# Performance work log

Hardware: AMD Instinct MI355X
Metric: run time of the kernel (lower is better)

Reference implementation:

```python
import math
import jax, jax.numpy as jnp
import numpy as np

NUM_HEADS = 12
NUM_LANDMARKS = 32

def iterative_inv(mat, n_iter=6):
    # mat: [B, H, m, m] row-stochastic kernel; Newton-Schulz pseudo-inverse
    m = mat.shape[-1]
    I = jnp.eye(m, dtype=mat.dtype)
    K = mat
    # 'else' branch: per-(B,H) normalization by max column sum
    denom = jnp.max(jnp.sum(K, axis=-2), axis=-1)[..., None, None]
    V = jnp.swapaxes(K, -1, -2) / denom
    for _ in range(n_iter):
        KV = jnp.matmul(K, V)
        V = jnp.matmul(0.25 * V, 13.0 * I - jnp.matmul(KV, 15.0 * I - jnp.matmul(KV, 7.0 * I - KV)))
    return V

def setup_inputs() -> dict:
    key = jax.random.key(0)
    k1, k2, k3 = jax.random.split(key, 3)
    B, N, C = 8, 2048, 768
    x = jax.random.normal(k1, (B, N, C), dtype=jnp.float32)
    w_qkv = jax.random.normal(k2, (C, 3 * C), dtype=jnp.float32) * (1.0 / math.sqrt(C))
    w_proj = jax.random.normal(k3, (C, C), dtype=jnp.float32) * (1.0 / math.sqrt(C))
    b_proj = jnp.zeros((C,), dtype=jnp.float32)
    return {"x": x, "w_qkv": w_qkv, "w_proj": w_proj, "b_proj": b_proj}

def reference(x, w_qkv, w_proj, b_proj):
    B, N, C = x.shape
    H = NUM_HEADS
    d = C // H
    m = NUM_LANDMARKS
    qkv = (x @ w_qkv).reshape(B, N, 3, H, d).transpose(2, 0, 3, 1, 4)  # [3,B,H,N,d]
    Q, K, V = qkv[0], qkv[1], qkv[2]
    scale = 1.0 / math.sqrt(math.sqrt(d))
    Q = Q * scale
    K = K * scale
    # landmark pooling: mean over contiguous chunks of size N//m
    Q_l = Q.reshape(B, H, m, N // m, d).mean(axis=-2)  # [B,H,m,d]
    K_l = K.reshape(B, H, m, N // m, d).mean(axis=-2)
    kernel_1 = jax.nn.softmax(jnp.einsum('bhnd,bhmd->bhnm', Q, K_l), axis=-1)   # [B,H,N,m]
    kernel_2 = jax.nn.softmax(jnp.einsum('bhmd,bhkd->bhmk', Q_l, K_l), axis=-1) # [B,H,m,m]
    kernel_3 = jax.nn.softmax(jnp.einsum('bhmd,bhnd->bhmn', Q_l, K), axis=-1)   # [B,H,m,N]
    X = jnp.matmul(jnp.matmul(kernel_1, iterative_inv(kernel_2)), jnp.matmul(kernel_3, V))  # [B,H,N,d]
    X = X.transpose(0, 2, 1, 3).reshape(B, N, C)
    return X @ w_proj + b_proj
```

## Files before the change

kernel.cpp:

```cpp
#include <hip/hip_runtime.h>
#include <hip/hip_bf16.h>

typedef __hip_bfloat16 bf16;
typedef __attribute__((ext_vector_type(8))) __bf16 bf16x8;
typedef __attribute__((ext_vector_type(4))) float f32x4;

#define NB 8
#define SEQ 2048
#define CH 768
#define NH 12
#define HD 64
#define NL 32
#define BHT (NB*NH)
#define TOK (NB*SEQ)
#define QK_SCALE 0.35355339059327379f

__device__ __forceinline__ void async_ld16(const bf16* g, bf16* l) {
    unsigned loff = (unsigned)__builtin_amdgcn_readfirstlane((int)(unsigned)(uintptr_t)l);
    __builtin_amdgcn_global_load_lds(
        (const __attribute__((address_space(1))) unsigned*)(uintptr_t)g,
        (__attribute__((address_space(3))) unsigned*)(uintptr_t)loff, 16, 0, 0);
}

__global__ void convert_x(const float* __restrict__ x, bf16* __restrict__ xb) {
    size_t i = ((size_t)blockIdx.x * 256 + threadIdx.x) * 8;
    float4 a = *reinterpret_cast<const float4*>(x + i);
    float4 b = *reinterpret_cast<const float4*>(x + i + 4);
    alignas(16) bf16 tmp[8];
    tmp[0] = __float2bfloat16(a.x); tmp[1] = __float2bfloat16(a.y);
    tmp[2] = __float2bfloat16(a.z); tmp[3] = __float2bfloat16(a.w);
    tmp[4] = __float2bfloat16(b.x); tmp[5] = __float2bfloat16(b.y);
    tmp[6] = __float2bfloat16(b.z); tmp[7] = __float2bfloat16(b.w);
    *reinterpret_cast<uint4*>(xb + i) = *reinterpret_cast<const uint4*>(tmp);
}

__global__ void transpose_f32(const float* __restrict__ in, bf16* __restrict__ outp,
                              int Hrows, int Wcols) {
    __shared__ float tile[32][33];
    int bx = blockIdx.x * 32, by = blockIdx.y * 32;
    int tx = threadIdx.x, ty = threadIdx.y;
    for (int i = 0; i < 32; i += 8)
        tile[ty + i][tx] = in[(size_t)(by + ty + i) * Wcols + bx + tx];
    __syncthreads();
    for (int i = 0; i < 32; i += 8)
        outp[(size_t)(bx + ty + i) * Hrows + by + tx] = __float2bfloat16(tile[tx][ty + i]);
}

template <int EPI>
__global__ __launch_bounds__(256) void gemm_bt(
    const bf16* __restrict__ A, const bf16* __restrict__ Bt,
    int Nout, int Kdim,
    bf16* __restrict__ q, bf16* __restrict__ k, bf16* __restrict__ vt,
    float* __restrict__ Ql, float* __restrict__ Kl,
    float* __restrict__ outp, const float* __restrict__ bias_f) {
    __shared__ __align__(16) bf16 As[128 * 32];
    __shared__ __align__(16) bf16 Bs[128 * 32];
    const int t = threadIdx.x;
    const int wave = t >> 6, lane = t & 63;
    const int quad = lane >> 4, l15 = lane & 15;
    const int wr = wave >> 1, wc = wave & 1;

    int p = blockIdx.y * gridDim.x + blockIdx.x;
    int xcd = p & 7, j = p >> 3;
    int gx = gridDim.x;
    int bn = j % gx;
    int bm = (j / gx) * 8 + xcd;
    const int bm0 = bm * 128;
    const int bn0 = bn * 128;

    f32x4 acc[4][4];
    const f32x4 zero4 = {0.f, 0.f, 0.f, 0.f};
    for (int i = 0; i < 4; i++)
        for (int jj = 0; jj < 4; jj++) acc[i][jj] = zero4;

    const int sw = (quad ^ (l15 & 3)) * 8;

    for (int k0 = 0; k0 < Kdim; k0 += 32) {
        __syncthreads();
        #pragma unroll
        for (int r = 0; r < 2; r++) {
            int c = t + r * 256;
            int row = c >> 2;
            int chunk = ((c & 3) ^ (row & 3)) * 8;
            async_ld16(&A[(size_t)(bm0 + row) * Kdim + k0 + chunk], &As[(wave * 64 + r * 256) * 8]);
            async_ld16(&Bt[(size_t)(bn0 + row) * Kdim + k0 + chunk], &Bs[(wave * 64 + r * 256) * 8]);
        }
        __syncthreads();
        bf16x8 af[4], bfr[4];
        #pragma unroll
        for (int mi = 0; mi < 4; mi++)
            af[mi] = *reinterpret_cast<const bf16x8*>(&As[(wr * 64 + mi * 16 + l15) * 32 + sw]);
        #pragma unroll
        for (int ni = 0; ni < 4; ni++)
            bfr[ni] = *reinterpret_cast<const bf16x8*>(&Bs[(wc * 64 + ni * 16 + l15) * 32 + sw]);
        #pragma unroll
        for (int mi = 0; mi < 4; mi++)
            #pragma unroll
            for (int ni = 0; ni < 4; ni++)
                acc[mi][ni] = __builtin_amdgcn_mfma_f32_16x16x32_bf16(af[mi], bfr[ni], acc[mi][ni], 0, 0, 0);
    }

    if (EPI == 0) {
        const int which = bn0 / CH;
        const int rem0 = bn0 - which * CH + wc * 64;
        const int b = bm0 >> 11;
        const int nnb = (bm0 & 2047) + wr * 64;
        if (which < 2) {
            bf16* dstqk = (which == 0) ? q : k;
            float* dstl = (which == 0) ? Ql : Kl;
            const int l = nnb >> 6;
            #pragma unroll
            for (int ni = 0; ni < 4; ni++) {
                int rem = rem0 + ni * 16 + l15;
                int h = rem >> 6, dd = rem & 63;
                int bh = b * NH + h;
                float colsum = 0.f;
                #pragma unroll
                for (int mi = 0; mi < 4; mi++) {
                    int nn0 = nnb + mi * 16 + quad * 4;
                    #pragma unroll
                    for (int r = 0; r < 4; r++) {
                        float val = acc[mi][ni][r];
                        colsum += val;
                        dstqk[((size_t)bh * SEQ + nn0 + r) * HD + dd] = __float2bfloat16(val * QK_SCALE);
                    }
                }
                colsum += __shfl_xor(colsum, 16);
                colsum += __shfl_xor(colsum, 32);
                if (quad == 0)
                    dstl[((size_t)bh * NL + l) * HD + dd] = colsum * (QK_SCALE / 64.f);
            }
        } else {
            #pragma unroll
            for (int ni = 0; ni < 4; ni++) {
                int rem = rem0 + ni * 16 + l15;
                int h = rem >> 6, dd = rem & 63;
                int bh = b * NH + h;
                #pragma unroll
                for (int mi = 0; mi < 4; mi++) {
                    int nn0 = nnb + mi * 16 + quad * 4;
                    alignas(8) bf16 four[4];
                    #pragma unroll
                    for (int r = 0; r < 4; r++) four[r] = __float2bfloat16(acc[mi][ni][r]);
                    *reinterpret_cast<uint2*>(&vt[((size_t)bh * HD + dd) * SEQ + nn0]) =
                        *reinterpret_cast<const uint2*>(four);
                }
            }
        }
    } else {
        #pragma unroll
        for (int mi = 0; mi < 4; mi++)
            #pragma unroll
            for (int ni = 0; ni < 4; ni++) {
                int col = bn0 + wc * 64 + ni * 16 + l15;
                #pragma unroll
                for (int r = 0; r < 4; r++) {
                    int row = bm0 + wr * 64 + mi * 16 + quad * 4 + r;
                    outp[(size_t)row * Nout + col] = acc[mi][ni][r] + bias_f[col];
                }
            }
    }
}

__global__ __launch_bounds__(256) void k3_pv(const float* __restrict__ Ql,
                                             const bf16* __restrict__ Kb,
                                             const bf16* __restrict__ Vt,
                                             float* __restrict__ Opart,
                                             float* __restrict__ Spart) {
    __shared__ __align__(16) bf16 Pw[4][32 * 136];
    __shared__ __align__(16) float Ored[4][32 * 65];
    __shared__ float Sred[4 * 32];
    const int bh = blockIdx.x, cc = blockIdx.y;
    const int n0 = cc * 512;
    const int t = threadIdx.x;
    const int w = t >> 6, lane = t & 63;
    const int quad = lane >> 4, l15 = lane & 15;

    const bf16* Kbh = Kb + (size_t)bh * SEQ * HD;
    const bf16* Vtb = Vt + (size_t)bh * HD * SEQ;

    bf16x8 af[2][2];
    #pragma unroll
    for (int mt = 0; mt < 2; mt++)
        #pragma unroll
        for (int kh = 0; kh < 2; kh++) {
            const float* src = Ql + (size_t)bh * NL * HD + (mt * 16 + l15) * 64 + kh * 32 + quad * 8;
            alignas(16) bf16 tmp[8];
            #pragma unroll
            for (int jj = 0; jj < 8; jj++) tmp[jj] = __float2bfloat16(src[jj]);
            af[mt][kh] = *reinterpret_cast<const bf16x8*>(tmp);
        }

    const f32x4 zero4 = {0.f, 0.f, 0.f, 0.f};
    f32x4 oacc[2][4];
    #pragma unroll
    for (int mt = 0; mt < 2; mt++)
        #pragma unroll
        for (int nd = 0; nd < 4; nd++) oacc[mt][nd] = zero4;
    float rs[2][4];
    #pragma unroll
    for (int mt = 0; mt < 2; mt++)
        #pragma unroll
        for (int r = 0; r < 4; r++) rs[mt][r] = 0.f;

    bf16* Pme = &Pw[w][0];

    #pragma unroll
    for (int h = 0; h < 2; h++) {
        f32x4 sacc[2][4];
        #pragma unroll
        for (int mt = 0; mt < 2; mt++)
            #pragma unroll
            for (int nt = 0; nt < 4; nt++) sacc[mt][nt] = zero4;
        #pragma unroll
        for (int nt = 0; nt < 4; nt++) {
            int n = n0 + w * 128 + h * 64 + nt * 16 + l15;
            bf16x8 kf0 = *reinterpret_cast<const bf16x8*>(&Kbh[(size_t)n * HD + quad * 8]);
            bf16x8 kf1 = *reinterpret_cast<const bf16x8*>(&Kbh[(size_t)n * HD + 32 + quad * 8]);
            #pragma unroll
            for (int mt = 0; mt < 2; mt++) {
                sacc[mt][nt] = __builtin_amdgcn_mfma_f32_16x16x32_bf16(af[mt][0], kf0, sacc[mt][nt], 0, 0, 0);
                sacc[mt][nt] = __builtin_amdgcn_mfma_f32_16x16x32_bf16(af[mt][1], kf1, sacc[mt][nt], 0, 0, 0);
            }
        }
        #pragma unroll
        for (int mt = 0; mt < 2; mt++)
            #pragma unroll
            for (int nt = 0; nt < 4; nt++)
                #pragma unroll
                for (int r = 0; r < 4; r++) {
                    float pv = __expf(sacc[mt][nt][r]);
                    rs[mt][r] += pv;
                    int row = mt * 16 + quad * 4 + r;
                    Pme[row * 136 + h * 64 + nt * 16 + l15] = __float2bfloat16(pv);
                }
    }
    __asm__ __volatile__("s_waitcnt lgkmcnt(0)" ::: "memory");

    #pragma unroll
    for (int kt = 0; kt < 4; kt++) {
        bf16x8 pa[2];
        pa[0] = *reinterpret_cast<const bf16x8*>(&Pme[l15 * 136 + kt * 32 + quad * 8]);
        pa[1] = *reinterpret_cast<const bf16x8*>(&Pme[(16 + l15) * 136 + kt * 32 + quad * 8]);
        int kbase = n0 + w * 128 + kt * 32 + quad * 8;
        #pragma unroll
        for (int nd = 0; nd < 4; nd++) {
            bf16x8 bv = *reinterpret_cast<const bf16x8*>(&Vtb[(size_t)(nd * 16 + l15) * SEQ + kbase]);
            oacc[0][nd] = __builtin_amdgcn_mfma_f32_16x16x32_bf16(pa[0], bv, oacc[0][nd], 0, 0, 0);
            oacc[1][nd] = __builtin_amdgcn_mfma_f32_16x16x32_bf16(pa[1], bv, oacc[1][nd], 0, 0, 0);
        }
    }

    #pragma unroll
    for (int mt = 0; mt < 2; mt++)
        #pragma unroll
        for (int r = 0; r < 4; r++) {
            float v = rs[mt][r];
            #pragma unroll
            for (int o = 1; o < 16; o <<= 1) v += __shfl_xor(v, o);
            rs[mt][r] = v;
        }
    if (l15 == 0)
        #pragma unroll
        for (int mt = 0; mt < 2; mt++)
            #pragma unroll
            for (int r = 0; r < 4; r++)
                Sred[w * 32 + mt * 16 + quad * 4 + r] = rs[mt][r];
    #pragma unroll
    for (int mt = 0; mt < 2; mt++)
        #pragma unroll
        for (int nd = 0; nd < 4; nd++)
            #pragma unroll
            for (int r = 0; r < 4; r++)
                Ored[w][(mt * 16 + quad * 4 + r) * 65 + nd * 16 + l15] = oacc[mt][nd][r];
    __syncthreads();

    float* Op = Opart + ((size_t)bh * 4 + cc) * (NL * HD);
    for (int e = t; e < 2048; e += 256) {
        int m = e >> 6, dd = e & 63;
        Op[e] = Ored[0][m * 65 + dd] + Ored[1][m * 65 + dd] +
                Ored[2][m * 65 + dd] + Ored[3][m * 65 + dd];
    }
    if (t < 32)
        Spart[((size_t)bh * 4 + cc) * NL + t] = Sred[t] + Sred[32 + t] + Sred[64 + t] + Sred[96 + t];
}

__device__ inline void mm32(float* Cm, const float* Am, const float* Bm, int t) {
    for (int e = t; e < 1024; e += 256) {
        int i = e >> 5, jj = e & 31;
        float s = 0.f;
        #pragma unroll
        for (int kk = 0; kk < 32; kk++) s += Am[i * 32 + kk] * Bm[kk * 32 + jj];
        Cm[e] = s;
    }
}

__global__ __launch_bounds__(256) void newton_inv(const float* __restrict__ Ql,
                                                  const float* __restrict__ Kl,
                                                  const float* __restrict__ Opart,
                                                  const float* __restrict__ Spart,
                                                  float* __restrict__ W2) {
    __shared__ float K2[1024], Vv[1024], KV[1024], Ta[1024], Tb[1024];
    __shared__ float K3[2048];
    __shared__ float stot[32];
    __shared__ float red[32];
    __shared__ float denom_s;
    int bh = blockIdx.x;
    int t = threadIdx.x;
    const float* ql = Ql + (size_t)bh * NL * HD;
    const float* kl = Kl + (size_t)bh * NL * HD;

    if (t < 32) {
        const float* sp = Spart + (size_t)bh * 4 * NL;
        stot[t] = sp[t] + sp[32 + t] + sp[64 + t] + sp[96 + t];
    }
    {
        const float* op = Opart + (size_t)bh * 4 * (NL * HD);
        for (int e = t; e < 2048; e += 256)
            K3[e] = op[e] + op[2048 + e] + op[4096 + e] + op[6144 + e];
    }

    for (int e = t; e < 1024; e += 256) {
        int i = e >> 5, jj = e & 31;
        float s = 0.f;
        #pragma unroll 8
        for (int d = 0; d < 64; d++) s += ql[i * 64 + d] * kl[jj * 64 + d];
        K2[e] = s;
    }
    __syncthreads();
    for (int e = t; e < 2048; e += 256) K3[e] *= (1.f / stot[e >> 6]);
    if (t < 32) {
        float mx = -1e30f;
        for (int jj = 0; jj < 32; jj++) mx = fmaxf(mx, K2[t * 32 + jj]);
        float sm = 0.f;
        for (int jj = 0; jj < 32; jj++) { float e = __expf(K2[t * 32 + jj] - mx); K2[t * 32 + jj] = e; sm += e; }
        float inv = 1.f / sm;
        for (int jj = 0; jj < 32; jj++) K2[t * 32 + jj] *= inv;
    }
    __syncthreads();
    if (t < 32) {
        float cs = 0.f;
        for (int i = 0; i < 32; i++) cs += K2[i * 32 + t];
        red[t] = cs;
    }
    __syncthreads();
    if (t == 0) {
        float mx = red[0];
        for (int jj = 1; jj < 32; jj++) mx = fmaxf(mx, red[jj]);
        denom_s = mx;
    }
    __syncthreads();
    float invden = 1.f / denom_s;
    for (int e = t; e < 1024; e += 256) {
        int i = e >> 5, jj = e & 31;
        Vv[e] = K2[jj * 32 + i] * invden;
    }
    __syncthreads();
    for (int it = 0; it < 6; it++) {
        mm32(KV, K2, Vv, t);
        __syncthreads();
        for (int e = t; e < 1024; e += 256) { int i = e >> 5, jj = e & 31; Ta[e] = ((i == jj) ? 7.f : 0.f) - KV[e]; }
        __syncthreads();
        mm32(Tb, KV, Ta, t);
        __syncthreads();
        for (int e = t; e < 1024; e += 256) { int i = e >> 5, jj = e & 31; Tb[e] = ((i == jj) ? 15.f : 0.f) - Tb[e]; }
        __syncthreads();
        mm32(Ta, KV, Tb, t);
        __syncthreads();
        for (int e = t; e < 1024; e += 256) { int i = e >> 5, jj = e & 31; Ta[e] = ((i == jj) ? 13.f : 0.f) - Ta[e]; }
        __syncthreads();
        mm32(Tb, Vv, Ta, t);
        __syncthreads();
        for (int e = t; e < 1024; e += 256) Vv[e] = 0.25f * Tb[e];
        __syncthreads();
    }
    for (int e = t; e < 2048; e += 256) {
        int i = e >> 6, dd = e & 63;
        float s = 0.f;
        #pragma unroll
        for (int kk = 0; kk < 32; kk++) s += Vv[i * 32 + kk] * K3[kk * 64 + dd];
        W2[(size_t)bh * NL * HD + e] = s;
    }
}

__global__ __launch_bounds__(256) void rows_fused(const bf16* __restrict__ Qb,
                                                  const float* __restrict__ Kl,
                                                  const float* __restrict__ W2,
                                                  bf16* __restrict__ Xp) {
    __shared__ __align__(16) bf16 Klb[32 * 64];
    __shared__ __align__(16) bf16 W2t[64 * 32];
    __shared__ __align__(16) bf16 Pw[4][32 * 40];
    const int bh = blockIdx.x, tile = blockIdx.y;
    const int t = threadIdx.x, w = t >> 6, lane = t & 63;
    const int quad = lane >> 4, l15 = lane & 15;

    {
        const float* ksrc = Kl + (size_t)bh * NL * HD;
        const float* wsrc = W2 + (size_t)bh * NL * HD;
        int e0 = t * 8;
        #pragma unroll
        for (int jj = 0; jj < 8; jj++) {
            int e = e0 + jj;
            Klb[e] = __float2bfloat16(ksrc[e]);
            int kk = e >> 6, dd = e & 63;
            W2t[dd * 32 + kk] = __float2bfloat16(wsrc[e]);
        }
    }
    __syncthreads();

    const int b = bh / NH, h = bh - b * NH;
    const int row0 = tile * 128 + w * 32;
    const bf16* qbase = Qb + ((size_t)bh * SEQ + row0) * HD;

    const f32x4 zero4 = {0.f, 0.f, 0.f, 0.f};
    f32x4 sacc[2][2];
    #pragma unroll
    for (int mt = 0; mt < 2; mt++)
        #pragma unroll
        for (int nt = 0; nt < 2; nt++) sacc[mt][nt] = zero4;
    #pragma unroll
    for (int kh = 0; kh < 2; kh++) {
        bf16x8 bk0 = *reinterpret_cast<const bf16x8*>(&Klb[(l15) * 64 + kh * 32 + quad * 8]);
        bf16x8 bk1 = *reinterpret_cast<const bf16x8*>(&Klb[(16 + l15) * 64 + kh * 32 + quad * 8]);
        #pragma unroll
        for (int mt = 0; mt < 2; mt++) {
            bf16x8 aq = *reinterpret_cast<const bf16x8*>(&qbase[(size_t)(mt * 16 + l15) * HD + kh * 32 + quad * 8]);
            sacc[mt][0] = __builtin_amdgcn_mfma_f32_16x16x32_bf16(aq, bk0, sacc[mt][0], 0, 0, 0);
            sacc[mt][1] = __builtin_amdgcn_mfma_f32_16x16x32_bf16(aq, bk1, sacc[mt][1], 0, 0, 0);
        }
    }

    float invs[2][4];
    bf16* Pme = &Pw[w][0];
    #pragma unroll
    for (int mt = 0; mt < 2; mt++)
        #pragma unroll
        for (int r = 0; r < 4; r++) {
            float v0 = __expf(sacc[mt][0][r]);
            float v1 = __expf(sacc[mt][1][r]);
            int row = mt * 16 + quad * 4 + r;
            Pme[row * 40 + l15] = __float2bfloat16(v0);
            Pme[row * 40 + 16 + l15] = __float2bfloat16(v1);
            float v = v0 + v1;
            #pragma unroll
            for (int o = 1; o < 16; o <<= 1) v += __shfl_xor(v, o);
            invs[mt][r] = 1.f / v;
        }
    __asm__ __volatile__("s_waitcnt lgkmcnt(0)" ::: "memory");

    f32x4 oacc[2][4];
    #pragma unroll
    for (int mt = 0; mt < 2; mt++)
        #pragma unroll
        for (int nd = 0; nd < 4; nd++) oacc[mt][nd] = zero4;
    bf16x8 pa[2];
    pa[0] = *reinterpret_cast<const bf16x8*>(&Pme[l15 * 40 + quad * 8]);
    pa[1] = *reinterpret_cast<const bf16x8*>(&Pme[(16 + l15) * 40 + quad * 8]);
    #pragma unroll
    for (int nd = 0; nd < 4; nd++) {
        bf16x8 bw = *reinterpret_cast<const bf16x8*>(&W2t[(nd * 16 + l15) * 32 + quad * 8]);
        oacc[0][nd] = __builtin_amdgcn_mfma_f32_16x16x32_bf16(pa[0], bw, oacc[0][nd], 0, 0, 0);
        oacc[1][nd] = __builtin_amdgcn_mfma_f32_16x16x32_bf16(pa[1], bw, oacc[1][nd], 0, 0, 0);
    }

    #pragma unroll
    for (int mt = 0; mt < 2; mt++)
        #pragma unroll
        for (int nd = 0; nd < 4; nd++)
            #pragma unroll
            for (int r = 0; r < 4; r++) {
                int row = row0 + mt * 16 + quad * 4 + r;
                Xp[((size_t)(b * SEQ + row)) * CH + h * 64 + nd * 16 + l15] =
                    __float2bfloat16(oacc[mt][nd][r] * invs[mt][r]);
            }
}

extern "C" void kernel_launch(void* const* d_in, const int* in_sizes, int n_in,
                              void* d_out, int out_size, void* d_ws, size_t ws_size,
                              hipStream_t stream) {
    const float* x      = (const float*)d_in[0];
    const float* w_qkv  = (const float*)d_in[1];
    const float* w_proj = (const float*)d_in[2];
    const float* b_proj = (const float*)d_in[3];
    float* out = (float*)d_out;

    char* ws = (char*)d_ws;
    size_t off = 0;
    auto alloc = [&](size_t bytes) -> void* {
        void* p = ws + off;
        off += (bytes + 255) & ~(size_t)255;
        return p;
    };
    bf16* wqkvT  = (bf16*)alloc((size_t)3 * CH * CH * 2);
    bf16* wprojT = (bf16*)alloc((size_t)CH * CH * 2);
    bf16* Qb     = (bf16*)alloc((size_t)BHT * SEQ * HD * 2);
    bf16* Kb     = (bf16*)alloc((size_t)BHT * SEQ * HD * 2);
    bf16* Vt     = (bf16*)alloc((size_t)BHT * SEQ * HD * 2);
    float* Ql    = (float*)alloc((size_t)BHT * NL * HD * 4);
    float* Kl    = (float*)alloc((size_t)BHT * NL * HD * 4);
    float* Opart = (float*)alloc((size_t)BHT * 4 * NL * HD * 4);
    float* Spart = (float*)alloc((size_t)BHT * 4 * NL * 4);
    float* W2    = (float*)alloc((size_t)BHT * NL * HD * 4);
    bf16* Xp     = (bf16*)alloc((size_t)TOK * CH * 2);
    if (ws_size < off) return;
    bf16* xb = Xp;

    convert_x<<<TOK * CH / 2048, 256, 0, stream>>>(x, xb);
    transpose_f32<<<dim3((3 * CH) / 32, CH / 32), dim3(32, 8), 0, stream>>>(w_qkv, wqkvT, CH, 3 * CH);
    transpose_f32<<<dim3(CH / 32, CH / 32), dim3(32, 8), 0, stream>>>(w_proj, wprojT, CH, CH);

    gemm_bt<0><<<dim3((3 * CH) / 128, TOK / 128), 256, 0, stream>>>(
        xb, wqkvT, 3 * CH, CH, Qb, Kb, Vt, Ql, Kl, nullptr, nullptr);

    k3_pv<<<dim3(BHT, 4), 256, 0, stream>>>(Ql, Kb, Vt, Opart, Spart);
    newton_inv<<<BHT, 256, 0, stream>>>(Ql, Kl, Opart, Spart, W2);
    rows_fused<<<dim3(BHT, SEQ / 128), 256, 0, stream>>>(Qb, Kl, W2, Xp);

    gemm_bt<1><<<dim3(CH / 128, TOK / 128), 256, 0, stream>>>(
        Xp, wprojT, CH, CH, nullptr, nullptr, nullptr, nullptr, nullptr, out, b_proj);
}
```

Measured before the change: 282.0 us.

## Rewrite GEMM as 256x256 tile, 8-wave, double-buffered pipelined kernel

Replaces the 128x128 single-buffered GEMM (BK=32) with a 256x256 tile, 512-thread, BK=64 kernel. It double-buffers LDS with async global-to-LDS loads staged in quarters interleaved with MFMA phases, uses s_setprio around the MFMA blocks, and adds an 8-way XOR swizzle. The goal is to hide load latency and improve data reuse for both the QKV and projection GEMMs. The cost is heavy register and LDS use (128KB LDS) and far fewer blocks: the projection GEMM gets only 3x64 = 192 blocks, which may underfill the 256 CUs.

```diff
diff --git a/kernel.cpp b/kernel.cpp
--- a/kernel.cpp
+++ b/kernel.cpp
@@ -14,6 +14,10 @@
 #define BHT (NB*NH)
 #define TOK (NB*SEQ)
 #define QK_SCALE 0.35355339059327379f
+
+#define BAR() __builtin_amdgcn_s_barrier()
+#define WLGKM0() __asm__ __volatile__("s_waitcnt lgkmcnt(0)" ::: "memory")
+#define WVM(n) __asm__ __volatile__("s_waitcnt vmcnt(" #n ")" ::: "memory")
 
 __device__ __forceinline__ void async_ld16(const bf16* g, bf16* l) {
     unsigned loff = (unsigned)__builtin_amdgcn_readfirstlane((int)(unsigned)(uintptr_t)l);
@@ -47,97 +51,192 @@
 }
 
 template <int EPI>
-__global__ __launch_bounds__(256) void gemm_bt(
+__global__ __launch_bounds__(512, 2) void gemm_bt(
     const bf16* __restrict__ A, const bf16* __restrict__ Bt,
     int Nout, int Kdim,
     bf16* __restrict__ q, bf16* __restrict__ k, bf16* __restrict__ vt,
     float* __restrict__ Ql, float* __restrict__ Kl,
     float* __restrict__ outp, const float* __restrict__ bias_f) {
-    __shared__ __align__(16) bf16 As[128 * 32];
-    __shared__ __align__(16) bf16 Bs[128 * 32];
+    __shared__ __align__(16) bf16 As[2][256 * 64];
+    __shared__ __align__(16) bf16 Bs[2][256 * 64];
     const int t = threadIdx.x;
     const int wave = t >> 6, lane = t & 63;
     const int quad = lane >> 4, l15 = lane & 15;
-    const int wr = wave >> 1, wc = wave & 1;
+    const int wr = wave >> 2, wc = wave & 3;
 
     int p = blockIdx.y * gridDim.x + blockIdx.x;
     int xcd = p & 7, j = p >> 3;
     int gx = gridDim.x;
     int bn = j % gx;
     int bm = (j / gx) * 8 + xcd;
-    const int bm0 = bm * 128;
-    const int bn0 = bn * 128;
-
-    f32x4 acc[4][4];
+    const int bm0 = bm * 256;
+    const int bn0 = bn * 256;
+
+    const int T = Kdim >> 6;
+
+    const int srow = t >> 3;
+    const int scol = (((t & 7) ^ (srow & 7)) << 3);
+    const bf16* Abase = A + (size_t)(bm0 + srow) * Kdim + scol;
+    const bf16* Bbase = Bt + (size_t)(bn0 + srow) * Kdim + scol;
+
+    auto stageA = [&](int kt, int hf) {
+        const bf16* g = Abase + (size_t)(hf * 128) * Kdim + kt * 64;
+        bf16* l = &As[kt & 1][hf * 8192 + t * 8];
+        async_ld16(g, l);
+        async_ld16(g + (size_t)64 * Kdim, l + 4096);
+    };
+    auto stageB = [&](int kt, int hf) {
+        const bf16* g = Bbase + (size_t)(hf * 128) * Kdim + kt * 64;
+        bf16* l = &Bs[kt & 1][hf * 8192 + t * 8];
+        async_ld16(g, l);
+        async_ld16(g + (size_t)64 * Kdim, l + 4096);
+    };
+
+    const int swk[2] = { (quad ^ (l15 & 7)) << 3, ((4 + quad) ^ (l15 & 7)) << 3 };
+    const bf16* arow = &As[0][wr * 8192 + l15 * 64];
+    const bf16* brow = &Bs[0][(wc >> 1) * 8192 + ((wc & 1) * 64 + l15) * 64];
+
+    f32x4 acc[8][4];
     const f32x4 zero4 = {0.f, 0.f, 0.f, 0.f};
-    for (int i = 0; i < 4; i++)
+    #pragma unroll
+    for (int i = 0; i < 8; i++)
+        #pragma unroll
         for (int jj = 0; jj < 4; jj++) acc[i][jj] = zero4;
 
-    const int sw = (quad ^ (l15 & 3)) * 8;
-
-    for (int k0 = 0; k0 < Kdim; k0 += 32) {
-        __syncthreads();
-        #pragma unroll
-        for (int r = 0; r < 2; r++) {
-            int c = t + r * 256;
-            int row = c >> 2;
-            int chunk = ((c & 3) ^ (row & 3)) * 8;
-            async_ld16(&A[(size_t)(bm0 + row) * Kdim + k0 + chunk], &As[(wave * 64 + r * 256) * 8]);
-            async_ld16(&Bt[(size_t)(bn0 + row) * Kdim + k0 + chunk], &Bs[(wave * 64 + r * 256) * 8]);
-        }
-        __syncthreads();
-        bf16x8 af[4], bfr[4];
+    stageA(0, 0); stageA(0, 1); stageB(0, 0); stageB(0, 1);
+    if (T > 1) {
+        stageB(1, 0); stageB(1, 1);
+        WVM(4);
+    } else {
+        WVM(0);
+    }
+    BAR();
+
+    bf16x8 a[4][2], b[4][2];
+    #pragma unroll 2
+    for (int kt = 0; kt < T; kt++) {
+        const int cur = kt & 1;
+        const bf16* ab = arow + cur * 16384;
+        const bf16* bb = brow + cur * 16384;
+
         #pragma unroll
         for (int mi = 0; mi < 4; mi++)
-            af[mi] = *reinterpret_cast<const bf16x8*>(&As[(wr * 64 + mi * 16 + l15) * 32 + sw]);
-        #pragma unroll
-        for (int ni = 0; ni < 4; ni++)
-            bfr[ni] = *reinterpret_cast<const bf16x8*>(&Bs[(wc * 64 + ni * 16 + l15) * 32 + sw]);
+            #pragma unroll
+            for (int kk = 0; kk < 2; kk++)
+                a[mi][kk] = *reinterpret_cast<const bf16x8*>(ab + mi * 1024 + swk[kk]);
+        #pragma unroll
+        for (int ni = 0; ni < 2; ni++)
+            #pragma unroll
+            for (int kk = 0; kk < 2; kk++)
+                b[ni][kk] = *reinterpret_cast<const bf16x8*>(bb + ni * 1024 + swk[kk]);
+        if (kt + 1 < T) stageA(kt + 1, 0);
+        BAR(); WLGKM0();
+        __builtin_amdgcn_s_setprio(1);
         #pragma unroll
         for (int mi = 0; mi < 4; mi++)
             #pragma unroll
-            for (int ni = 0; ni < 4; ni++)
-                acc[mi][ni] = __builtin_amdgcn_mfma_f32_16x16x32_bf16(af[mi], bfr[ni], acc[mi][ni], 0, 0, 0);
+            for (int ni = 0; ni < 2; ni++)
+                #pragma unroll
+                for (int kk = 0; kk < 2; kk++)
+                    acc[mi][ni] = __builtin_amdgcn_mfma_f32_16x16x32_bf16(a[mi][kk], b[ni][kk], acc[mi][ni], 0, 0, 0);
+        __builtin_amdgcn_s_setprio(0);
+        BAR();
+
+        #pragma unroll
+        for (int ni = 2; ni < 4; ni++)
+            #pragma unroll
+            for (int kk = 0; kk < 2; kk++)
+                b[ni][kk] = *reinterpret_cast<const bf16x8*>(bb + ni * 1024 + swk[kk]);
+        if (kt + 1 < T) stageA(kt + 1, 1);
+        BAR(); WLGKM0();
+        __builtin_amdgcn_s_setprio(1);
+        #pragma unroll
+        for (int mi = 0; mi < 4; mi++)
+            #pragma unroll
+            for (int ni = 2; ni < 4; ni++)
+                #pragma unroll
+                for (int kk = 0; kk < 2; kk++)
+                    acc[mi][ni] = __builtin_amdgcn_mfma_f32_16x16x32_bf16(a[mi][kk], b[ni][kk], acc[mi][ni], 0, 0, 0);
+        __builtin_amdgcn_s_setprio(0);
+        BAR();
+
+        #pragma unroll
+        for (int mi = 0; mi < 4; mi++)
+            #pragma unroll
+            for (int kk = 0; kk < 2; kk++)
+                a[mi][kk] = *reinterpret_cast<const bf16x8*>(ab + (mi + 4) * 1024 + swk[kk]);
+        if (kt + 2 < T) stageB(kt + 2, 0);
+        BAR(); WLGKM0();
+        __builtin_amdgcn_s_setprio(1);
+        #pragma unroll
+        for (int mi = 0; mi < 4; mi++)
+            #pragma unroll
+            for (int ni = 0; ni < 2; ni++)
+                #pragma unroll
+                for (int kk = 0; kk < 2; kk++)
+                    acc[mi + 4][ni] = __builtin_amdgcn_mfma_f32_16x16x32_bf16(a[mi][kk], b[ni][kk], acc[mi + 4][ni], 0, 0, 0);
+        __builtin_amdgcn_s_setprio(0);
+        BAR();
+
+        if (kt + 2 < T) stageB(kt + 2, 1);
+        BAR(); WLGKM0();
+        __builtin_amdgcn_s_setprio(1);
+        #pragma unroll
+        for (int mi = 0; mi < 4; mi++)
+            #pragma unroll
+            for (int ni = 2; ni < 4; ni++)
+                #pragma unroll
+                for (int kk = 0; kk < 2; kk++)
+                    acc[mi + 4][ni] = __builtin_amdgcn_mfma_f32_16x16x32_bf16(a[mi][kk], b[ni][kk], acc[mi + 4][ni], 0, 0, 0);
+        __builtin_amdgcn_s_setprio(0);
+        if (kt + 2 < T) {
+            WVM(4);
+        } else if (kt + 1 < T) {
+            WVM(0);
+        }
+        BAR();
     }
 
     if (EPI == 0) {
         const int which = bn0 / CH;
         const int rem0 = bn0 - which * CH + wc * 64;
         const int b = bm0 >> 11;
-        const int nnb = (bm0 & 2047) + wr * 64;
+        const int h = rem0 >> 6;
+        const int bh = b * NH + h;
+        const int nnb = (bm0 & 2047) + wr * 128;
         if (which < 2) {
             bf16* dstqk = (which == 0) ? q : k;
             float* dstl = (which == 0) ? Ql : Kl;
-            const int l = nnb >> 6;
-            #pragma unroll
-            for (int ni = 0; ni < 4; ni++) {
-                int rem = rem0 + ni * 16 + l15;
-                int h = rem >> 6, dd = rem & 63;
-                int bh = b * NH + h;
-                float colsum = 0.f;
-                #pragma unroll
-                for (int mi = 0; mi < 4; mi++) {
-                    int nn0 = nnb + mi * 16 + quad * 4;
+            const int la0 = nnb >> 6;
+            #pragma unroll
+            for (int hf = 0; hf < 2; hf++) {
+                #pragma unroll
+                for (int ni = 0; ni < 4; ni++) {
+                    int dd = ni * 16 + l15;
+                    float colsum = 0.f;
                     #pragma unroll
-                    for (int r = 0; r < 4; r++) {
-                        float val = acc[mi][ni][r];
-                        colsum += val;
-                        dstqk[((size_t)bh * SEQ + nn0 + r) * HD + dd] = __float2bfloat16(val * QK_SCALE);
+                    for (int m2 = 0; m2 < 4; m2++) {
+                        int mi = hf * 4 + m2;
+                        int nn0 = nnb + mi * 16 + quad * 4;
+                        #pragma unroll
+                        for (int r = 0; r < 4; r++) {
+                            float val = acc[mi][ni][r];
+                            colsum += val;
+                            dstqk[((size_t)bh * SEQ + nn0 + r) * HD + dd] = __float2bfloat16(val * QK_SCALE);
+                        }
                     }
+                    colsum += __shfl_xor(colsum, 16);
+                    colsum += __shfl_xor(colsum, 32);
+                    if (quad == 0)
+                        dstl[((size_t)bh * NL + la0 + hf) * HD + dd] = colsum * (QK_SCALE / 64.f);
                 }
-                colsum += __shfl_xor(colsum, 16);
-                colsum += __shfl_xor(colsum, 32);
-                if (quad == 0)
-                    dstl[((size_t)bh * NL + l) * HD + dd] = colsum * (QK_SCALE / 64.f);
             }
         } else {
             #pragma unroll
             for (int ni = 0; ni < 4; ni++) {
-                int rem = rem0 + ni * 16 + l15;
-                int h = rem >> 6, dd = rem & 63;
-                int bh = b * NH + h;
-                #pragma unroll
-                for (int mi = 0; mi < 4; mi++) {
+                int dd = ni * 16 + l15;
+                #pragma unroll
+                for (int mi = 0; mi < 8; mi++) {
                     int nn0 = nnb + mi * 16 + quad * 4;
                     alignas(8) bf16 four[4];
                     #pragma unroll
@@ -149,16 +248,17 @@
         }
     } else {
         #pragma unroll
-        for (int mi = 0; mi < 4; mi++)
-            #pragma unroll
-            for (int ni = 0; ni < 4; ni++) {
-                int col = bn0 + wc * 64 + ni * 16 + l15;
+        for (int ni = 0; ni < 4; ni++) {
+            int col = bn0 + wc * 64 + ni * 16 + l15;
+            float bb = bias_f[col];
+            #pragma unroll
+            for (int mi = 0; mi < 8; mi++)
                 #pragma unroll
                 for (int r = 0; r < 4; r++) {
-                    int row = bm0 + wr * 64 + mi * 16 + quad * 4 + r;
-                    outp[(size_t)row * Nout + col] = acc[mi][ni][r] + bias_f[col];
+                    int row = bm0 + wr * 128 + mi * 16 + quad * 4 + r;
+                    outp[(size_t)row * Nout + col] = acc[mi][ni][r] + bb;
                 }
-            }
+        }
     }
 }
 
@@ -509,13 +609,13 @@
     transpose_f32<<<dim3((3 * CH) / 32, CH / 32), dim3(32, 8), 0, stream>>>(w_qkv, wqkvT, CH, 3 * CH);
     transpose_f32<<<dim3(CH / 32, CH / 32), dim3(32, 8), 0, stream>>>(w_proj, wprojT, CH, CH);
 
-    gemm_bt<0><<<dim3((3 * CH) / 128, TOK / 128), 256, 0, stream>>>(
+    gemm_bt<0><<<dim3((3 * CH) / 256, TOK / 256), 512, 0, stream>>>(
         xb, wqkvT, 3 * CH, CH, Qb, Kb, Vt, Ql, Kl, nullptr, nullptr);
 
     k3_pv<<<dim3(BHT, 4), 256, 0, stream>>>(Ql, Kb, Vt, Opart, Spart);
     newton_inv<<<BHT, 256, 0, stream>>>(Ql, Kl, Opart, Spart, W2);
     rows_fused<<<dim3(BHT, SEQ / 128), 256, 0, stream>>>(Qb, Kl, W2, Xp);
 
-    gemm_bt<1><<<dim3(CH / 128, TOK / 128), 256, 0, stream>>>(
+    gemm_bt<1><<<dim3(CH / 256, TOK / 256), 512, 0, stream>>>(
         Xp, wprojT, CH, CH, nullptr, nullptr, nullptr, nullptr, nullptr, out, b_proj);
 }
```

Result: no change. 284.3 us (+0.8%).
